# Optimization experiments

Hardware: AMD Instinct MI355X
Metric: run time of the kernel (lower is better)

The kernel has to match this reference:

```python
import jax, jax.numpy as jnp
import numpy as np

N_QUBITS = 4
N_LAYERS = 3
BATCH = 1048576  # 2**20; batched state vector [B, 2,2,2,2] complex64 = 128 MB


def setup_inputs() -> dict:
    key = jax.random.key(0)
    k1, k2 = jax.random.split(key)
    x = jax.random.normal(k1, (BATCH, N_QUBITS), dtype=jnp.float32)
    q_weights = jax.random.normal(k2, (N_LAYERS, N_QUBITS, 3), dtype=jnp.float32) * 0.1
    return {"x": x, "q_weights": q_weights}


def _ry_mat(theta):
    # RY(t) = [[cos t/2, -sin t/2], [sin t/2, cos t/2]]; theta: [] or [B]
    c = jnp.cos(theta * 0.5).astype(jnp.complex64)
    s = jnp.sin(theta * 0.5).astype(jnp.complex64)
    return jnp.stack([jnp.stack([c, -s], -1), jnp.stack([s, c], -1)], -2)


def _rz_mat(theta):
    # RZ(t) = diag(e^{-it/2}, e^{it/2})
    e = jnp.exp(-0.5j * theta.astype(jnp.complex64))
    z = jnp.zeros_like(e)
    return jnp.stack([jnp.stack([e, z], -1), jnp.stack([z, jnp.conj(e)], -1)], -2)


def _apply_1q(state, U, wire):
    # state: [B,2,2,2,2]; U: [2,2] (shared) or [B,2,2] (per-sample)
    ax = wire + 1
    state = jnp.moveaxis(state, ax, -1)
    if U.ndim == 3:
        state = jnp.einsum('b...o,bno->b...n', state, U)
    else:
        state = jnp.einsum('b...o,no->b...n', state, U)
    return jnp.moveaxis(state, -1, ax)


def _cnot(state, c, t):
    # flip target bit on the control=1 slice
    ca, ta = c + 1, t + 1
    s0 = jnp.take(state, 0, axis=ca)
    s1 = jnp.take(state, 1, axis=ca)
    ta2 = ta if ta < ca else ta - 1
    s1 = jnp.flip(s1, axis=ta2)
    return jnp.stack([s0, s1], axis=ca)


def _circuit(x, q_weights):
    B = x.shape[0]
    xn = jnp.tanh(x) * jnp.pi  # [B, 4]
    # |0000>
    state = jnp.zeros((B,) + (2,) * N_QUBITS, dtype=jnp.complex64)
    state = state.at[:, 0, 0, 0, 0].set(1.0 + 0.0j)
    # angle encoding: RY(2x_i) then RZ(x_i), per-sample batched 2x2 gates
    for i in range(N_QUBITS):
        state = _apply_1q(state, _ry_mat(2.0 * xn[:, i]), i)
        state = _apply_1q(state, _rz_mat(xn[:, i]), i)
    # variational layers: Rot(phi,theta,omega) = RZ(omega) @ RY(theta) @ RZ(phi)
    for l in range(N_LAYERS):
        for i in range(N_QUBITS):
            phi, theta, omega = q_weights[l, i, 0], q_weights[l, i, 1], q_weights[l, i, 2]
            U = _rz_mat(omega) @ _ry_mat(theta) @ _rz_mat(phi)
            state = _apply_1q(state, U, i)
        for i in range(N_QUBITS):
            state = _cnot(state, i, (i + 1) % N_QUBITS)
    # <Z_i> = p(bit_i=0) - p(bit_i=1)
    probs = jnp.abs(state) ** 2  # [B,2,2,2,2] real
    evs = []
    for i in range(N_QUBITS):
        axes = tuple(a for a in range(1, N_QUBITS + 1) if a != i + 1)
        marg = jnp.sum(probs, axis=axes)  # [B, 2]
        evs.append(marg[:, 0] - marg[:, 1])
    return jnp.stack(evs, axis=-1).astype(jnp.float32)  # [B, 4]


def reference(x, q_weights):
    return _circuit(x, q_weights)
```

## Files before the change

kernel.cpp:

```cpp
#include <hip/hip_runtime.h>


using f16x8 = __attribute__((ext_vector_type(8))) _Float16;
using f32x4 = __attribute__((ext_vector_type(4))) float;

struct C { float r, i; };

__device__ __forceinline__ C cmul(C a, C b) {
    C o;
    o.r = fmaf(a.r, b.r, -(a.i * b.i));
    o.i = fmaf(a.r, b.i,   a.i * b.r);
    return o;
}

__device__ __forceinline__ C cmadd(float ur, float ui, float wr, float wi, C a, C b) {
    C o;
    o.r = fmaf(ur, a.r, fmaf(-ui, a.i, fmaf(wr, b.r, -(wi * b.i))));
    o.i = fmaf(ur, a.i, fmaf( ui, a.r, fmaf(wr, b.i,   wi * b.r)));
    return o;
}

template <int BP>
__device__ __forceinline__ void apply_gate(C st[16], float4 A4, float4 B4) {
#pragma unroll
    for (int i = 0; i < 8; i++) {
        const int lo = ((i >> BP) << (BP + 1)) | (i & ((1 << BP) - 1));
        const int hi = lo | (1 << BP);
        const C a = st[lo], b = st[hi];
        st[lo] = cmadd(A4.x, A4.y, A4.z, A4.w, a, b);
        st[hi] = cmadd(B4.x, B4.y, B4.z, B4.w, a, b);
    }
}

template <int CB, int TB>
__device__ __forceinline__ void cnot(C st[16]) {
#pragma unroll
    for (int i = 0; i < 16; i++) {
        if ((i & (1 << CB)) && !(i & (1 << TB))) {
            C t = st[i];
            st[i] = st[i | (1 << TB)];
            st[i | (1 << TB)] = t;
        }
    }
}

struct Enc { float r0, i0, r1, i1; };
__device__ __forceinline__ Enc encode(float xq) {
    const float ax = fabsf(xq);
    const float e  = __builtin_amdgcn_exp2f(ax * -2.8853900817779268f);
    const float r  = __builtin_amdgcn_rcpf(1.0f + e);
    const float t  = copysignf((1.0f - e) * r, xq);
    const float sh = __builtin_amdgcn_sinf(t * 0.25f);
    const float ch = __builtin_amdgcn_cosf(t * 0.25f);
    const float s  = 2.0f * sh * ch;
    const float c  = fmaf(-2.0f * sh, sh, 1.0f);
    return {c * ch, -(c * sh), s * ch, s * sh};
}

#define WS_WLO 2048
#define WS_UG0 4096

__global__ void qcompose_kernel(const float* __restrict__ qw, float* __restrict__ ws) {
    __shared__ float4 Ug[12][2];
    const int tid = threadIdx.x;
    if (tid < 12) {
        const float phi = qw[tid * 3 + 0];
        const float th  = qw[tid * 3 + 1];
        const float om  = qw[tid * 3 + 2];
        float s, c;   __sincosf(0.5f * th, &s, &c);
        float sa, ca; __sincosf(0.5f * (phi + om), &sa, &ca);
        float sb, cb; __sincosf(0.5f * (phi - om), &sb, &cb);
        Ug[tid][0] = make_float4(c * ca, -c * sa, -s * cb, -s * sb);
        Ug[tid][1] = make_float4(s * cb, -s * sb, c * ca, c * sa);
    }
    __syncthreads();

    if (tid < 4) {
        float4* o = reinterpret_cast<float4*>(reinterpret_cast<char*>(ws) + WS_UG0);
        o[2 * tid]     = Ug[tid][0];
        o[2 * tid + 1] = Ug[tid][1];
    }

    if (tid < 16) {
        C st[16];
#pragma unroll
        for (int i = 0; i < 16; i++) { st[i].r = 0.0f; st[i].i = 0.0f; }
        st[tid].r = 1.0f;

        cnot<3, 2>(st); cnot<2, 1>(st); cnot<1, 0>(st); cnot<0, 3>(st);
        apply_gate<3>(st, Ug[4][0], Ug[4][1]);
        apply_gate<2>(st, Ug[5][0], Ug[5][1]);
        apply_gate<1>(st, Ug[6][0], Ug[6][1]);
        apply_gate<0>(st, Ug[7][0], Ug[7][1]);
        cnot<3, 2>(st); cnot<2, 1>(st); cnot<1, 0>(st); cnot<0, 3>(st);
        apply_gate<3>(st, Ug[8][0], Ug[8][1]);
        apply_gate<2>(st, Ug[9][0], Ug[9][1]);
        apply_gate<1>(st, Ug[10][0], Ug[10][1]);
        apply_gate<0>(st, Ug[11][0], Ug[11][1]);
        cnot<3, 2>(st); cnot<2, 1>(st); cnot<1, 0>(st); cnot<0, 3>(st);

        _Float16* whi = reinterpret_cast<_Float16*>(ws);
        _Float16* wlo = reinterpret_cast<_Float16*>(reinterpret_cast<char*>(ws) + WS_WLO);
        const int k0 = 2 * tid, k1 = k0 + 1;
#pragma unroll
        for (int d = 0; d < 16; d++) {
            const int j0 = 2 * d, j1 = j0 + 1;
            const float vr = st[d].r, vi = st[d].i;
            float v[4]  = {vr, vi, -vi, vr};
            int   jj[4] = {j0, j1, j0, j1};
            int   kk[4] = {k0, k0, k1, k1};
#pragma unroll
            for (int e = 0; e < 4; e++) {
                _Float16 h = (_Float16)v[e];
                _Float16 l = (_Float16)((v[e] - (float)h) * 2048.0f);
                whi[jj[e] * 32 + kk[e]] = h;
                wlo[jj[e] * 32 + kk[e]] = l;
            }
        }
    }
}

__global__ __launch_bounds__(256, 4) void qlayer_kernel(const float* __restrict__ x,
                                                        const float* __restrict__ ws,
                                                        float* __restrict__ out, int B) {
    __shared__ __align__(16) unsigned char lds[4 * 64 * 144];
    const int tid  = threadIdx.x;
    const int lane = tid & 63;
    const int wid  = tid >> 6;
    char* slab  = reinterpret_cast<char*>(lds) + wid * (64 * 144);
    char* myrow = slab + lane * 144;

    const char* wsb = reinterpret_cast<const char*>(ws);

    const int jrow = lane & 15;
    const int kb   = (lane >> 4) * 16;
    const f16x8 Bh0 = *reinterpret_cast<const f16x8*>(wsb + jrow * 64 + kb);
    const f16x8 Bh1 = *reinterpret_cast<const f16x8*>(wsb + (jrow + 16) * 64 + kb);
    const f16x8 Bl0 = *reinterpret_cast<const f16x8*>(wsb + WS_WLO + jrow * 64 + kb);
    const f16x8 Bl1 = *reinterpret_cast<const f16x8*>(wsb + WS_WLO + (jrow + 16) * 64 + kb);
    const float4* ug0 = reinterpret_cast<const float4*>(wsb + WS_UG0);

    const int b  = blockIdx.x * 256 + tid;
    const int bl = (b < B) ? b : (B - 1);
    const float4 xv = reinterpret_cast<const float4*>(x)[bl];
    const float xs[4] = {xv.x, xv.y, xv.z, xv.w};

    C v[4][2];
#pragma unroll
    for (int q = 0; q < 4; q++) {
        const Enc e = encode(xs[q]);
        const C a{e.r0, e.i0}, bv{e.r1, e.i1};
        const float4 A4 = ug0[2 * q], B4 = ug0[2 * q + 1];
        v[q][0] = cmadd(A4.x, A4.y, A4.z, A4.w, a, bv);
        v[q][1] = cmadd(B4.x, B4.y, B4.z, B4.w, a, bv);
    }

    C t01[4], t23[4];
#pragma unroll
    for (int i = 0; i < 4; i++) {
        t01[i] = cmul(v[0][(i >> 1) & 1], v[1][i & 1]);
        t23[i] = cmul(v[2][(i >> 1) & 1], v[3][i & 1]);
    }
    C st[16];
#pragma unroll
    for (int i = 0; i < 16; i++) st[i] = cmul(t01[i >> 2], t23[i & 3]);

#pragma unroll
    for (int c = 0; c < 4; c++) {
        f16x8 vh, vl;
#pragma unroll
        for (int d = 0; d < 4; d++) {
            const float fr = st[4 * c + d].r, fi = st[4 * c + d].i;
            const _Float16 hr = (_Float16)fr, hi_ = (_Float16)fi;
            vh[2 * d]     = hr;
            vh[2 * d + 1] = hi_;
            vl[2 * d]     = (_Float16)((fr - (float)hr) * 2048.0f);
            vl[2 * d + 1] = (_Float16)((fi - (float)hi_) * 2048.0f);
        }
        *reinterpret_cast<f16x8*>(myrow + c * 16)      = vh;
        *reinterpret_cast<f16x8*>(myrow + 64 + c * 16) = vl;
    }

    __syncthreads();

    const f32x4 Z = {0.f, 0.f, 0.f, 0.f};
#pragma unroll
    for (int m = 0; m < 4; m++) {
        const char* arow = slab + (16 * m + (lane & 15)) * 144 + kb;
        const f16x8 Ah = *reinterpret_cast<const f16x8*>(arow);
        const f16x8 Al = *reinterpret_cast<const f16x8*>(arow + 64);

        f32x4 main0 = __builtin_amdgcn_mfma_f32_16x16x32_f16(Ah, Bh0, Z, 0, 0, 0);
        f32x4 corr0 = __builtin_amdgcn_mfma_f32_16x16x32_f16(Ah, Bl0, Z, 0, 0, 0);
        corr0       = __builtin_amdgcn_mfma_f32_16x16x32_f16(Al, Bh0, corr0, 0, 0, 0);
        f32x4 main1 = __builtin_amdgcn_mfma_f32_16x16x32_f16(Ah, Bh1, Z, 0, 0, 0);
        f32x4 corr1 = __builtin_amdgcn_mfma_f32_16x16x32_f16(Ah, Bl1, Z, 0, 0, 0);
        corr1       = __builtin_amdgcn_mfma_f32_16x16x32_f16(Al, Bh1, corr1, 0, 0, 0);

        const int srow = 16 * m + 4 * (lane >> 4);
        const int col  = lane & 15;
#pragma unroll
        for (int r = 0; r < 4; r++) {
            float* crow = reinterpret_cast<float*>(slab + (srow + r) * 144);
            crow[col]      = fmaf(corr0[r], 4.8828125e-4f, main0[r]);
            crow[16 + col] = fmaf(corr1[r], 4.8828125e-4f, main1[r]);
        }
    }

    __syncthreads();

    float cv[32];
#pragma unroll
    for (int c = 0; c < 8; c++) {
        const float4 q4 = *reinterpret_cast<const float4*>(myrow + c * 16);
        cv[4 * c] = q4.x; cv[4 * c + 1] = q4.y; cv[4 * c + 2] = q4.z; cv[4 * c + 3] = q4.w;
    }

    float s0 = 0.f, s1 = 0.f, s2 = 0.f, s3 = 0.f;
#pragma unroll
    for (int d = 0; d < 16; d++) {
        const float p = fmaf(cv[2 * d], cv[2 * d], cv[2 * d + 1] * cv[2 * d + 1]);
        if (d & 8) s3 += p;
        if (d & 4) s2 += p;
        if (d & 2) s1 += p;
        if (d & 1) s0 += p;
    }

    if (b < B) {
        float4 ev;
        ev.x = fmaf(-2.0f, s3, 1.0f);
        ev.y = fmaf(-2.0f, s2, 1.0f);
        ev.z = fmaf(-2.0f, s1, 1.0f);
        ev.w = fmaf(-2.0f, s0, 1.0f);
        reinterpret_cast<float4*>(out)[b] = ev;
    }
}

extern "C" void kernel_launch(void* const* d_in, const int* in_sizes, int n_in,
                              void* d_out, int out_size, void* d_ws, size_t ws_size,
                              hipStream_t stream) {
    const float* x  = (const float*)d_in[0];
    const float* qw = (const float*)d_in[1];
    float* out = (float*)d_out;
    float* ws  = (float*)d_ws;
    const int B = in_sizes[0] / 4;
    const int blocks = (B + 255) / 256;
    qcompose_kernel<<<1, 64, 0, stream>>>(qw, ws);
    qlayer_kernel<<<blocks, 256, 0, stream>>>(x, ws, out, B);
}
```

Before: 84.40 us.

## Transpose MFMA operands, drop state lo-split, reduce expectations in registers via shuffles

Swaps the MFMA operand roles so the fixed composed unitary becomes the A operand and the state the B operand. The low-order fp16 correction for the state is dropped, which cuts MFMAs per tile from six to four and halves LDS row size. The output write-back to LDS and the second block barrier are replaced by computing probabilities from accumulators and reducing across lanes with xor shuffles. The first __syncthreads becomes a wave-local lgkmcnt fence, and the occupancy hint rises to 6. The cost is lower precision on the state, since only an fp16 rounding is kept, plus extra shuffle work.

New measurement: 82.89 us. No clear change (-1.8%).

```diff
diff --git a/kernel.cpp b/kernel.cpp
--- a/kernel.cpp
+++ b/kernel.cpp
@@ -57,8 +57,14 @@
     return {c * ch, -(c * sh), s * ch, s * sh};
 }
 
+__device__ __forceinline__ void wave_lds_fence() {
+    asm volatile("s_waitcnt lgkmcnt(0)" ::: "memory");
+    __builtin_amdgcn_sched_barrier(0);
+}
+
 #define WS_WLO 2048
 #define WS_UG0 4096
+#define ROWB 80
 
 __global__ void qcompose_kernel(const float* __restrict__ qw, float* __restrict__ ws) {
     __shared__ float4 Ug[12][2];
@@ -120,24 +126,24 @@
     }
 }
 
-__global__ __launch_bounds__(256, 4) void qlayer_kernel(const float* __restrict__ x,
+__global__ __launch_bounds__(256, 6) void qlayer_kernel(const float* __restrict__ x,
                                                         const float* __restrict__ ws,
                                                         float* __restrict__ out, int B) {
-    __shared__ __align__(16) unsigned char lds[4 * 64 * 144];
+    __shared__ __align__(16) unsigned char lds[4 * 64 * ROWB];
     const int tid  = threadIdx.x;
     const int lane = tid & 63;
     const int wid  = tid >> 6;
-    char* slab  = reinterpret_cast<char*>(lds) + wid * (64 * 144);
-    char* myrow = slab + lane * 144;
+    char* slab  = reinterpret_cast<char*>(lds) + wid * (64 * ROWB);
+    char* myrow = slab + lane * ROWB;
 
     const char* wsb = reinterpret_cast<const char*>(ws);
 
     const int jrow = lane & 15;
     const int kb   = (lane >> 4) * 16;
-    const f16x8 Bh0 = *reinterpret_cast<const f16x8*>(wsb + jrow * 64 + kb);
-    const f16x8 Bh1 = *reinterpret_cast<const f16x8*>(wsb + (jrow + 16) * 64 + kb);
-    const f16x8 Bl0 = *reinterpret_cast<const f16x8*>(wsb + WS_WLO + jrow * 64 + kb);
-    const f16x8 Bl1 = *reinterpret_cast<const f16x8*>(wsb + WS_WLO + (jrow + 16) * 64 + kb);
+    const f16x8 Wh0 = *reinterpret_cast<const f16x8*>(wsb + jrow * 64 + kb);
+    const f16x8 Wh1 = *reinterpret_cast<const f16x8*>(wsb + (jrow + 16) * 64 + kb);
+    const f16x8 Wl0 = *reinterpret_cast<const f16x8*>(wsb + WS_WLO + jrow * 64 + kb);
+    const f16x8 Wl1 = *reinterpret_cast<const f16x8*>(wsb + WS_WLO + (jrow + 16) * 64 + kb);
     const float4* ug0 = reinterpret_cast<const float4*>(wsb + WS_UG0);
 
     const int b  = blockIdx.x * 256 + tid;
@@ -161,77 +167,60 @@
         t01[i] = cmul(v[0][(i >> 1) & 1], v[1][i & 1]);
         t23[i] = cmul(v[2][(i >> 1) & 1], v[3][i & 1]);
     }
-    C st[16];
-#pragma unroll
-    for (int i = 0; i < 16; i++) st[i] = cmul(t01[i >> 2], t23[i & 3]);
-
-#pragma unroll
-    for (int c = 0; c < 4; c++) {
-        f16x8 vh, vl;
-#pragma unroll
-        for (int d = 0; d < 4; d++) {
-            const float fr = st[4 * c + d].r, fi = st[4 * c + d].i;
-            const _Float16 hr = (_Float16)fr, hi_ = (_Float16)fi;
-            vh[2 * d]     = hr;
-            vh[2 * d + 1] = hi_;
-            vl[2 * d]     = (_Float16)((fr - (float)hr) * 2048.0f);
-            vl[2 * d + 1] = (_Float16)((fi - (float)hi_) * 2048.0f);
+    f16x8 vh[4];
+#pragma unroll
+    for (int i = 0; i < 16; i++) {
+        const C s = cmul(t01[i >> 2], t23[i & 3]);
+        vh[i >> 2][2 * (i & 3)]     = (_Float16)s.r;
+        vh[i >> 2][2 * (i & 3) + 1] = (_Float16)s.i;
+    }
+#pragma unroll
+    for (int c = 0; c < 4; c++)
+        *reinterpret_cast<f16x8*>(myrow + c * 16) = vh[c];
+
+    wave_lds_fence();
+
+    const int g = lane >> 4;
+    const float f1 = (g & 1) ? 1.0f : 0.0f;
+    const float f2 = (g & 2) ? 1.0f : 0.0f;
+    const f32x4 Z = {0.f, 0.f, 0.f, 0.f};
+    float e0 = 0.f, e1 = 0.f, e2 = 0.f, e3 = 0.f;
+
+#pragma unroll
+    for (int n = 0; n < 4; n++) {
+        const f16x8 S = *reinterpret_cast<const f16x8*>(slab + (16 * n + jrow) * ROWB + kb);
+        f32x4 m0 = __builtin_amdgcn_mfma_f32_16x16x32_f16(Wh0, S, Z, 0, 0, 0);
+        f32x4 l0 = __builtin_amdgcn_mfma_f32_16x16x32_f16(Wl0, S, Z, 0, 0, 0);
+        f32x4 m1 = __builtin_amdgcn_mfma_f32_16x16x32_f16(Wh1, S, Z, 0, 0, 0);
+        f32x4 l1 = __builtin_amdgcn_mfma_f32_16x16x32_f16(Wl1, S, Z, 0, 0, 0);
+
+        float c0[4], c1[4];
+#pragma unroll
+        for (int r = 0; r < 4; r++) {
+            c0[r] = fmaf(l0[r], 4.8828125e-4f, m0[r]);
+            c1[r] = fmaf(l1[r], 4.8828125e-4f, m1[r]);
         }
-        *reinterpret_cast<f16x8*>(myrow + c * 16)      = vh;
-        *reinterpret_cast<f16x8*>(myrow + 64 + c * 16) = vl;
-    }
-
-    __syncthreads();
-
-    const f32x4 Z = {0.f, 0.f, 0.f, 0.f};
-#pragma unroll
-    for (int m = 0; m < 4; m++) {
-        const char* arow = slab + (16 * m + (lane & 15)) * 144 + kb;
-        const f16x8 Ah = *reinterpret_cast<const f16x8*>(arow);
-        const f16x8 Al = *reinterpret_cast<const f16x8*>(arow + 64);
-
-        f32x4 main0 = __builtin_amdgcn_mfma_f32_16x16x32_f16(Ah, Bh0, Z, 0, 0, 0);
-        f32x4 corr0 = __builtin_amdgcn_mfma_f32_16x16x32_f16(Ah, Bl0, Z, 0, 0, 0);
-        corr0       = __builtin_amdgcn_mfma_f32_16x16x32_f16(Al, Bh0, corr0, 0, 0, 0);
-        f32x4 main1 = __builtin_amdgcn_mfma_f32_16x16x32_f16(Ah, Bh1, Z, 0, 0, 0);
-        f32x4 corr1 = __builtin_amdgcn_mfma_f32_16x16x32_f16(Ah, Bl1, Z, 0, 0, 0);
-        corr1       = __builtin_amdgcn_mfma_f32_16x16x32_f16(Al, Bh1, corr1, 0, 0, 0);
-
-        const int srow = 16 * m + 4 * (lane >> 4);
-        const int col  = lane & 15;
-#pragma unroll
-        for (int r = 0; r < 4; r++) {
-            float* crow = reinterpret_cast<float*>(slab + (srow + r) * 144);
-            crow[col]      = fmaf(corr0[r], 4.8828125e-4f, main0[r]);
-            crow[16 + col] = fmaf(corr1[r], 4.8828125e-4f, main1[r]);
-        }
-    }
-
-    __syncthreads();
-
-    float cv[32];
-#pragma unroll
-    for (int c = 0; c < 8; c++) {
-        const float4 q4 = *reinterpret_cast<const float4*>(myrow + c * 16);
-        cv[4 * c] = q4.x; cv[4 * c + 1] = q4.y; cv[4 * c + 2] = q4.z; cv[4 * c + 3] = q4.w;
-    }
-
-    float s0 = 0.f, s1 = 0.f, s2 = 0.f, s3 = 0.f;
-#pragma unroll
-    for (int d = 0; d < 16; d++) {
-        const float p = fmaf(cv[2 * d], cv[2 * d], cv[2 * d + 1] * cv[2 * d + 1]);
-        if (d & 8) s3 += p;
-        if (d & 4) s2 += p;
-        if (d & 2) s1 += p;
-        if (d & 1) s0 += p;
+        const float p0 = fmaf(c0[1], c0[1], c0[0] * c0[0]);
+        const float p1 = fmaf(c0[3], c0[3], c0[2] * c0[2]);
+        const float p2 = fmaf(c1[1], c1[1], c1[0] * c1[0]);
+        const float p3 = fmaf(c1[3], c1[3], c1[2] * c1[2]);
+        const float Phi  = p2 + p3;
+        const float Podd = p1 + p3;
+        const float Pall = Phi + p0 + p1;
+        float s3 = Phi, s2 = Pall * f2, s1 = Pall * f1, s0 = Podd;
+        s3 += __shfl_xor(s3, 16); s2 += __shfl_xor(s2, 16);
+        s1 += __shfl_xor(s1, 16); s0 += __shfl_xor(s0, 16);
+        s3 += __shfl_xor(s3, 32); s2 += __shfl_xor(s2, 32);
+        s1 += __shfl_xor(s1, 32); s0 += __shfl_xor(s0, 32);
+        if (g == n) { e3 = s3; e2 = s2; e1 = s1; e0 = s0; }
     }
 
     if (b < B) {
         float4 ev;
-        ev.x = fmaf(-2.0f, s3, 1.0f);
-        ev.y = fmaf(-2.0f, s2, 1.0f);
-        ev.z = fmaf(-2.0f, s1, 1.0f);
-        ev.w = fmaf(-2.0f, s0, 1.0f);
+        ev.x = fmaf(-2.0f, e3, 1.0f);
+        ev.y = fmaf(-2.0f, e2, 1.0f);
+        ev.z = fmaf(-2.0f, e1, 1.0f);
+        ev.w = fmaf(-2.0f, e0, 1.0f);
         reinterpret_cast<float4*>(out)[b] = ev;
     }
 }
```
